# Optimization experiments

Measured on AMD Instinct MI355X. Metric: run time of the kernel, lower is better.

## Reference

```python
import jax, jax.numpy as jnp
import numpy as np

L_LAYERS = 4
N_HEAD = 16
D_MODEL = 1024
D_K = 64
D_V = 64
D_HID = 4096
D_OUT = 10000
SEQ = 512
BATCH = 16
MASK_RATE = 0.15
LN_EPS = 1e-5


def sinusoid_table(n_position, model_size):
    pos = np.arange(n_position)[:, None]
    hid = np.arange(model_size)[None, :]
    angle = pos / np.power(10000, 2 * (hid // 2) / model_size)
    tab = np.array(angle)
    tab[:, 0::2] = np.sin(tab[:, 0::2])
    tab[:, 1::2] = np.cos(tab[:, 1::2])
    return jnp.asarray(tab, dtype=jnp.float32)


def layer_norm(x, w, b):
    mu = jnp.mean(x, axis=-1, keepdims=True)
    var = jnp.mean(jnp.square(x - mu), axis=-1, keepdims=True)
    return (x - mu) * jax.lax.rsqrt(var + LN_EPS) * w + b


def setup_inputs() -> dict:
    key = jax.random.key(0)
    ks = jax.random.split(key, 32)
    s = 0.02
    inp = {
        "x": jax.random.normal(ks[0], (SEQ, BATCH, D_MODEL), dtype=jnp.float32),
        "rnd": jax.random.uniform(ks[1], (BATCH, SEQ), dtype=jnp.float32),
        "posi": sinusoid_table(SEQ, D_MODEL),
        "ln0_w": jnp.ones((D_MODEL,), jnp.float32),
        "ln0_b": jnp.zeros((D_MODEL,), jnp.float32),
        # stacked per-layer params [L, ...]
        "Wq": jax.random.normal(ks[2], (L_LAYERS, N_HEAD * D_K, D_MODEL), jnp.float32) * np.sqrt(2.0 / (D_MODEL + D_K)),
        "bq": jnp.zeros((L_LAYERS, N_HEAD * D_K), jnp.float32),
        "Wk": jax.random.normal(ks[3], (L_LAYERS, N_HEAD * D_K, D_MODEL), jnp.float32) * np.sqrt(2.0 / (D_MODEL + D_K)),
        "bk": jnp.zeros((L_LAYERS, N_HEAD * D_K), jnp.float32),
        "Wv": jax.random.normal(ks[4], (L_LAYERS, N_HEAD * D_V, D_MODEL), jnp.float32) * np.sqrt(2.0 / (D_MODEL + D_V)),
        "bv": jnp.zeros((L_LAYERS, N_HEAD * D_V), jnp.float32),
        "Wfc": jax.random.normal(ks[5], (L_LAYERS, D_MODEL, N_HEAD * D_V), jnp.float32) * s,
        "bfc": jnp.zeros((L_LAYERS, D_MODEL), jnp.float32),
        "ln1_w": jnp.ones((L_LAYERS, D_MODEL), jnp.float32),
        "ln1_b": jnp.zeros((L_LAYERS, D_MODEL), jnp.float32),
        "W1": jax.random.normal(ks[6], (L_LAYERS, D_HID, D_MODEL), jnp.float32) * s,
        "b1": jnp.zeros((L_LAYERS, D_HID), jnp.float32),
        "W2": jax.random.normal(ks[7], (L_LAYERS, D_MODEL, D_HID), jnp.float32) * s,
        "b2": jnp.zeros((L_LAYERS, D_MODEL), jnp.float32),
        "ln2_w": jnp.ones((L_LAYERS, D_MODEL), jnp.float32),
        "ln2_b": jnp.zeros((L_LAYERS, D_MODEL), jnp.float32),
        "Wo": jax.random.normal(ks[8], (D_OUT, D_MODEL), jnp.float32) * s,
        "bo": jnp.zeros((D_OUT,), jnp.float32),
    }
    return inp


def reference(x, rnd, posi, ln0_w, ln0_b, Wq, bq, Wk, bk, Wv, bv, Wfc, bfc,
              ln1_w, ln1_b, W1, b1, W2, b2, ln2_w, ln2_b, Wo, bo):
    scale = 1.0 / np.sqrt(D_K)
    # [length, batch, d] -> [batch, length, d]
    h = jnp.transpose(x, (1, 0, 2))
    # random input masking: keep where rnd > mask_rate
    keep = (rnd > MASK_RATE).astype(h.dtype)  # [B, S]
    h = h * keep[:, :, None]
    enc = layer_norm(h, ln0_w, ln0_b) + posi[None, :, :]

    for l in range(L_LAYERS):
        residual = enc
        q = (enc @ Wq[l].T + bq[l]).reshape(BATCH, SEQ, N_HEAD, D_K)
        k = (enc @ Wk[l].T + bk[l]).reshape(BATCH, SEQ, N_HEAD, D_K)
        v = (enc @ Wv[l].T + bv[l]).reshape(BATCH, SEQ, N_HEAD, D_V)
        attn = jnp.einsum('bqhd,bkhd->bhqk', q, k) * scale
        attn = jax.nn.softmax(attn, axis=-1)
        out = jnp.einsum('bhqk,bkhd->bqhd', attn, v).reshape(BATCH, SEQ, N_HEAD * D_V)
        out = out @ Wfc[l].T + bfc[l]
        enc = layer_norm(out + residual, ln1_w[l], ln1_b[l])
        # position-wise FFN (conv1d kernel=1 == per-token linear)
        ff = jax.nn.relu(enc @ W1[l].T + b1[l]) @ W2[l].T + b2[l]
        enc = layer_norm(ff + enc, ln2_w[l], ln2_b[l])

    logits = enc @ Wo.T + bo  # [B, S, D_OUT]
    out = jax.nn.log_softmax(logits, axis=-1)
    return jnp.transpose(out, (1, 0, 2))  # [S, B, D_OUT]
```

## Files before the change

### kernel.cpp

```cpp
#include <hip/hip_runtime.h>
#include <cstdint>

typedef unsigned short u16;
typedef unsigned int u32;
typedef __attribute__((ext_vector_type(8))) short vs8;
typedef __attribute__((ext_vector_type(4))) short vs4;
typedef __attribute__((ext_vector_type(4))) float vf4;
typedef __attribute__((ext_vector_type(4))) float f32x4;

#define NLAYER 4
#define SEQ 512
#define BATCH 16
#define DM 1024
#define NTOK 8192
#define DOUT 10000
#define DOUTP 10240

static __device__ __forceinline__ u16 f2bf(float f) {
    u32 u = __float_as_uint(f);
    return (u16)((u + 0x7FFFu + ((u >> 16) & 1u)) >> 16);
}
static __device__ __forceinline__ float bf2f(u16 h) { return __uint_as_float((u32)h << 16); }

static __device__ __forceinline__ void gload16(const void* g, void* l) {
    __builtin_amdgcn_global_load_lds(
        (const __attribute__((address_space(1))) u32*)(uintptr_t)g,
        (__attribute__((address_space(3))) u32*)(u32)(uintptr_t)l, 16, 0, 0);
}

template <int BM, bool RELU, bool OUTBF, bool TRV = false>
__global__ __launch_bounds__(512, 1) void gemm2p(const u16* __restrict__ A, const u16* __restrict__ Bw,
                                                 const float* __restrict__ bias, void* __restrict__ Cv,
                                                 int N, int K, int nMt, int nNt)
{
    constexpr int LA = BM / 128;
    constexpr int LB = 2;
    constexpr int WCNT = 2 * (LA + LB);
    constexpr int MR = BM / 32;

    __shared__ __align__(16) u16 lds[2 * 2 * BM * 32 + 2 * 2 * 256 * 32];
    u16* As = lds;
    u16* Bs = lds + 2 * 2 * BM * 32;

    const int t = threadIdx.x;
    const int wid = t >> 6, lane = t & 63;
    const int lr = lane & 15, lg = lane >> 4;
    const int wr = wid >> 2, wc = wid & 3;
    const int wrb = wr * (BM / 2), wcb = wc * 64;
    const int slot8 = (lg ^ ((lr >> 1) & 3)) * 8;

    const int nwg = nMt * nNt;
    const int orig = blockIdx.x;
    const int q8 = nwg >> 3, r8 = nwg & 7;
    const int xcd = orig & 7, idx = orig >> 3;
    const int wg = ((xcd < r8) ? xcd * (q8 + 1) : r8 * (q8 + 1) + (xcd - r8) * q8) + idx;
    const int GN = 8;
    const int gsz = GN * nMt;
    const int grp = wg / gsz;
    const int rem = wg - grp * gsz;
    const int gw = min(GN, nNt - grp * GN);
    const int mt = rem / gw;
    const int nt = grp * GN + (rem - mt * gw);
    const size_t m0 = (size_t)mt * BM;
    const size_t n0 = (size_t)nt * 256;

    const int srow = wid * 16 + (lane >> 2);
    const int scg = (lane & 3) ^ ((lane >> 3) & 3);
    const u16* gA = A + (m0 + srow) * (size_t)K + scg * 8;
    const u16* gB = Bw + (n0 + srow) * (size_t)K + scg * 8;

    auto stageA = [&](int b, int kh, int kt) {
#pragma unroll
        for (int i = 0; i < LA; ++i)
            gload16(gA + (size_t)i * 128 * K + kt + kh * 32,
                    &As[(((b << 1) + kh) * BM + (i * 8 + wid) * 16) * 32]);
    };
    auto stageB = [&](int b, int kh, int kt) {
#pragma unroll
        for (int i = 0; i < LB; ++i)
            gload16(gB + (size_t)i * 128 * K + kt + kh * 32,
                    &Bs[(((b << 1) + kh) * 256 + (i * 8 + wid) * 16) * 32]);
    };
    auto ldA = [&](int i, int kk, int b) -> vs8 {
        return *(const vs8*)&As[(((b << 1) + kk) * BM + wrb + i * 16 + lr) * 32 + slot8];
    };
    auto ldB = [&](int j, int kk, int b) -> vs8 {
        return *(const vs8*)&Bs[(((b << 1) + kk) * 256 + wcb + j * 16 + lr) * 32 + slot8];
    };

    f32x4 acc[MR][4];
#pragma unroll
    for (int i = 0; i < MR; ++i)
#pragma unroll
        for (int j = 0; j < 4; ++j) acc[i][j] = (f32x4){0.f, 0.f, 0.f, 0.f};

    const int NT = K >> 6;

    stageA(0, 0, 0); stageB(0, 0, 0);
    stageA(0, 1, 0); stageB(0, 1, 0);
    stageA(1, 0, 64); stageB(1, 0, 64);
    if constexpr (WCNT == 8) asm volatile("s_waitcnt vmcnt(8)" ::: "memory");
    else                     asm volatile("s_waitcnt vmcnt(6)" ::: "memory");
    __builtin_amdgcn_s_barrier();

    for (int tt = 0; tt < NT; ++tt) {
        const int buf = tt & 1;
        const int ktn = min(tt + 1, NT - 1) << 6;
        const int ktn2 = min(tt + 2, NT - 1) << 6;
        vs8 af[MR], bf[4];

#pragma unroll
        for (int j = 0; j < 4; ++j) bf[j] = ldB(j, 0, buf);
#pragma unroll
        for (int i = 0; i < MR; ++i) af[i] = ldA(i, 0, buf);
        stageA(buf ^ 1, 1, ktn);
        stageB(buf ^ 1, 1, ktn);
        __builtin_amdgcn_s_barrier();
        asm volatile("s_waitcnt lgkmcnt(0)" ::: "memory");
        __builtin_amdgcn_sched_barrier(0);
        __builtin_amdgcn_s_setprio(1);
#pragma unroll
        for (int i = 0; i < MR; ++i)
#pragma unroll
            for (int j = 0; j < 4; ++j) {
                if constexpr (TRV)
                    acc[i][j] = __builtin_amdgcn_mfma_f32_16x16x32_bf16(af[i], bf[j], acc[i][j], 0, 0, 0);
                else
                    acc[i][j] = __builtin_amdgcn_mfma_f32_16x16x32_bf16(bf[j], af[i], acc[i][j], 0, 0, 0);
            }
        __builtin_amdgcn_s_setprio(0);
        if constexpr (WCNT == 8) asm volatile("s_waitcnt vmcnt(8)" ::: "memory");
        else                     asm volatile("s_waitcnt vmcnt(6)" ::: "memory");
        __builtin_amdgcn_s_barrier();

#pragma unroll
        for (int j = 0; j < 4; ++j) bf[j] = ldB(j, 1, buf);
#pragma unroll
        for (int i = 0; i < MR; ++i) af[i] = ldA(i, 1, buf);
        stageA(buf, 0, ktn2);
        stageB(buf, 0, ktn2);
        __builtin_amdgcn_s_barrier();
        asm volatile("s_waitcnt lgkmcnt(0)" ::: "memory");
        __builtin_amdgcn_sched_barrier(0);
        __builtin_amdgcn_s_setprio(1);
#pragma unroll
        for (int i = 0; i < MR; ++i)
#pragma unroll
            for (int j = 0; j < 4; ++j) {
                if constexpr (TRV)
                    acc[i][j] = __builtin_amdgcn_mfma_f32_16x16x32_bf16(af[i], bf[j], acc[i][j], 0, 0, 0);
                else
                    acc[i][j] = __builtin_amdgcn_mfma_f32_16x16x32_bf16(bf[j], af[i], acc[i][j], 0, 0, 0);
            }
        __builtin_amdgcn_s_setprio(0);
        if constexpr (WCNT == 8) asm volatile("s_waitcnt vmcnt(8)" ::: "memory");
        else                     asm volatile("s_waitcnt vmcnt(6)" ::: "memory");
        __builtin_amdgcn_s_barrier();
    }

    asm volatile("s_waitcnt vmcnt(0)" ::: "memory");

    if constexpr (TRV) {
#pragma unroll
        for (int i = 0; i < MR; ++i) {
            const int cm0 = (int)m0 + wrb + 16 * i + lg * 4;
            const int b_ = cm0 >> 9, s_ = cm0 & 511;
#pragma unroll
            for (int j = 0; j < 4; ++j) {
                const int cn = (int)n0 + wcb + 16 * j + lr;
                const float bval = bias[cn];
                vs4 o;
#pragma unroll
                for (int r = 0; r < 4; ++r) o[r] = (short)f2bf(acc[i][j][r] + bval);
                u16* dst = (u16*)Cv + (((size_t)(b_ * 16 + (cn >> 6))) * 64 + (cn & 63)) * 512 + s_;
                *(vs4*)dst = o;
            }
        }
    } else {
#pragma unroll
        for (int i = 0; i < MR; ++i) {
            const size_t cm = m0 + wrb + 16 * i + lr;
#pragma unroll
            for (int j = 0; j < 4; ++j) {
                const size_t cn = n0 + wcb + 16 * j + lg * 4;
                const vf4 bv4 = *(const vf4*)&bias[cn];
                f32x4 v = acc[i][j];
#pragma unroll
                for (int r = 0; r < 4; ++r) {
                    v[r] += bv4[r];
                    if (RELU) v[r] = fmaxf(v[r], 0.f);
                }
                if (OUTBF) {
                    vs4 o;
#pragma unroll
                    for (int r = 0; r < 4; ++r) o[r] = (short)f2bf(v[r]);
                    *(vs4*)&((u16*)Cv)[cm * (size_t)N + cn] = o;
                } else {
                    *(vf4*)&((float*)Cv)[cm * (size_t)N + cn] = v;
                }
            }
        }
    }
}

__global__ __launch_bounds__(256) void attn_k(const u16* __restrict__ qb, const u16* __restrict__ kb,
                                              const u16* __restrict__ vtb, u16* __restrict__ ob, int ldq)
{
    __shared__ __align__(16) float SlF[32 * 520];
    const int t = threadIdx.x;
    const int wid = t >> 6, lane = t & 63;
    const int lr = lane & 15, lg = lane >> 4;
    const int bh = blockIdx.x >> 4, qt = blockIdx.x & 15;
    const int b = bh >> 4, h = bh & 15;
    const int q0 = qt * 32;

    vs8 aq[2][2];
#pragma unroll
    for (int i2 = 0; i2 < 2; ++i2)
#pragma unroll
        for (int kk = 0; kk < 2; ++kk)
            aq[i2][kk] = *(const vs8*)(qb + ((size_t)(b * 512 + q0 + 16 * i2 + lr)) * ldq + h * 64 + kk * 32 + lg * 8);

    f32x4 sa[2][8];
#pragma unroll
    for (int i2 = 0; i2 < 2; ++i2)
#pragma unroll
        for (int j = 0; j < 8; ++j) sa[i2][j] = (f32x4){0.f, 0.f, 0.f, 0.f};

#pragma unroll
    for (int j = 0; j < 8; ++j) {
        const int col = 128 * wid + 16 * j + lr;
#pragma unroll
        for (int kk = 0; kk < 2; ++kk) {
            vs8 bk = *(const vs8*)(kb + ((size_t)(b * 512 + col)) * ldq + h * 64 + kk * 32 + lg * 8);
#pragma unroll
            for (int i2 = 0; i2 < 2; ++i2)
                sa[i2][j] = __builtin_amdgcn_mfma_f32_16x16x32_bf16(bk, aq[i2][kk], sa[i2][j], 0, 0, 0);
        }
    }
#pragma unroll
    for (int i2 = 0; i2 < 2; ++i2)
#pragma unroll
        for (int j = 0; j < 8; ++j) {
            vf4 w;
#pragma unroll
            for (int r = 0; r < 4; ++r) w[r] = sa[i2][j][r] * 0.125f;
            *(vf4*)&SlF[(16 * i2 + lr) * 520 + 128 * wid + 16 * j + 4 * lg] = w;
        }
    __syncthreads();

    {
        const int row = t >> 3, seg = t & 7;
        const float* Sr = &SlF[row * 520 + seg * 64];
        float v[64];
        float m = -3.0e38f;
#pragma unroll
        for (int c = 0; c < 16; ++c) {
            const int cc = (c + row + seg) & 15;
            const vf4 w = *(const vf4*)&Sr[cc * 4];
#pragma unroll
            for (int e = 0; e < 4; ++e) { v[c * 4 + e] = w[e]; m = fmaxf(m, w[e]); }
        }
        m = fmaxf(m, __shfl_xor(m, 1));
        m = fmaxf(m, __shfl_xor(m, 2));
        m = fmaxf(m, __shfl_xor(m, 4));
        float s = 0.f;
#pragma unroll
        for (int i = 0; i < 64; ++i) { v[i] = __expf(v[i] - m); s += v[i]; }
        s += __shfl_xor(s, 1);
        s += __shfl_xor(s, 2);
        s += __shfl_xor(s, 4);
        const float inv = 1.f / s;
        u16* P16 = (u16*)SlF;
#pragma unroll
        for (int c = 0; c < 16; ++c) {
            const int cc = (c + row + seg) & 15;
            vs4 o;
#pragma unroll
            for (int e = 0; e < 4; ++e) o[e] = (short)f2bf(v[c * 4 + e] * inv);
            *(vs4*)&P16[row * 1040 + seg * 64 + cc * 4] = o;
        }
    }
    __syncthreads();

    const int rt = wid >> 1, ct0 = (wid & 1) * 2;
    f32x4 oa[2];
    oa[0] = (f32x4){0.f, 0.f, 0.f, 0.f};
    oa[1] = (f32x4){0.f, 0.f, 0.f, 0.f};
    const u16* P16 = (const u16*)SlF;
#pragma unroll
    for (int kt = 0; kt < 16; ++kt) {
        vs8 pa = *(const vs8*)&P16[(16 * rt + lr) * 1040 + kt * 32 + lg * 8];
#pragma unroll
        for (int c = 0; c < 2; ++c) {
            const int col = (ct0 + c) * 16 + lr;
            vs8 bv = *(const vs8*)(vtb + ((size_t)bh * 64 + col) * 512 + kt * 32 + lg * 8);
            oa[c] = __builtin_amdgcn_mfma_f32_16x16x32_bf16(bv, pa, oa[c], 0, 0, 0);
        }
    }
#pragma unroll
    for (int c = 0; c < 2; ++c) {
        const int qq = q0 + 16 * rt + lr;
        const int d0c = h * 64 + (ct0 + c) * 16 + lg * 4;
        vs4 o;
#pragma unroll
        for (int r = 0; r < 4; ++r) o[r] = (short)f2bf(oa[c][r]);
        *(vs4*)&ob[((size_t)b * 512 + qq) * 1024 + d0c] = o;
    }
}

__global__ __launch_bounds__(256) void embed_k(const float* __restrict__ x, const float* __restrict__ rnd,
                                               const float* __restrict__ posi, const float* __restrict__ w,
                                               const float* __restrict__ bb, u16* __restrict__ outb)
{
    const int tok = blockIdx.x;
    const int b = tok >> 9, s = tok & 511;
    const int t = threadIdx.x;
    const float keep = rnd[tok] > 0.15f ? 1.f : 0.f;
    vf4 xv = ((const vf4*)(x + ((size_t)s * 16 + b) * 1024))[t];
    xv *= keep;
    float s1 = xv[0] + xv[1] + xv[2] + xv[3];
    float s2 = xv[0] * xv[0] + xv[1] * xv[1] + xv[2] * xv[2] + xv[3] * xv[3];
#pragma unroll
    for (int mk = 1; mk < 64; mk <<= 1) { s1 += __shfl_xor(s1, mk); s2 += __shfl_xor(s2, mk); }
    __shared__ float red[8];
    if ((t & 63) == 0) { red[t >> 6] = s1; red[4 + (t >> 6)] = s2; }
    __syncthreads();
    s1 = red[0] + red[1] + red[2] + red[3];
    s2 = red[4] + red[5] + red[6] + red[7];
    const float mu = s1 * (1.f / 1024.f);
    const float var = s2 * (1.f / 1024.f) - mu * mu;
    const float rs = rsqrtf(var + 1e-5f);
    vf4 wv = ((const vf4*)w)[t];
    vf4 bv = ((const vf4*)bb)[t];
    vf4 pv = ((const vf4*)(posi + (size_t)s * 1024))[t];
    vs4 yb;
#pragma unroll
    for (int c = 0; c < 4; ++c)
        yb[c] = (short)f2bf((xv[c] - mu) * rs * wv[c] + bv[c] + pv[c]);
    *(vs4*)(outb + (size_t)tok * 1024 + t * 4) = yb;
}

__global__ __launch_bounds__(256) void add_ln_k(const u16* x, const u16* resid,
                                                const float* __restrict__ w, const float* __restrict__ bb,
                                                u16* out)
{
    const size_t row = blockIdx.x;
    const int t = threadIdx.x;
    const vs4 xv4 = *(const vs4*)(x + row * 1024 + t * 4);
    const vs4 rv4 = *(const vs4*)(resid + row * 1024 + t * 4);
    float xv[4];
#pragma unroll
    for (int c = 0; c < 4; ++c) xv[c] = bf2f((u16)xv4[c]) + bf2f((u16)rv4[c]);
    float s1 = xv[0] + xv[1] + xv[2] + xv[3];
    float s2 = xv[0] * xv[0] + xv[1] * xv[1] + xv[2] * xv[2] + xv[3] * xv[3];
#pragma unroll
    for (int mk = 1; mk < 64; mk <<= 1) { s1 += __shfl_xor(s1, mk); s2 += __shfl_xor(s2, mk); }
    __shared__ float red[8];
    if ((t & 63) == 0) { red[t >> 6] = s1; red[4 + (t >> 6)] = s2; }
    __syncthreads();
    s1 = red[0] + red[1] + red[2] + red[3];
    s2 = red[4] + red[5] + red[6] + red[7];
    const float mu = s1 * (1.f / 1024.f);
    const float var = s2 * (1.f / 1024.f) - mu * mu;
    const float rs = rsqrtf(var + 1e-5f);
    const vf4 wv = ((const vf4*)w)[t];
    const vf4 bv = ((const vf4*)bb)[t];
    vs4 yb;
#pragma unroll
    for (int c = 0; c < 4; ++c)
        yb[c] = (short)f2bf((xv[c] - mu) * rs * wv[c] + bv[c]);
    *(vs4*)(out + row * 1024 + t * 4) = yb;
}

__global__ __launch_bounds__(256) void logsm_k(const u16* __restrict__ lgts, float* __restrict__ out)
{
    const int tok = blockIdx.x;
    const int b = tok >> 9, s = tok & 511;
    const int t = threadIdx.x;
    const vs4* row4 = (const vs4*)(lgts + (size_t)tok * DOUTP);
    float v[40];
    float m = -3.0e38f;
#pragma unroll
    for (int i = 0; i < 10; ++i) {
        const int g = t + 256 * i;
        const vs4 x4 = __builtin_nontemporal_load(row4 + g);
#pragma unroll
        for (int e = 0; e < 4; ++e) {
            const float f = (g < 2500) ? bf2f((u16)x4[e]) : -3.0e38f;
            v[i * 4 + e] = f;
            m = fmaxf(m, f);
        }
    }
#pragma unroll
    for (int mk = 1; mk < 64; mk <<= 1) m = fmaxf(m, __shfl_xor(m, mk));
    __shared__ float red[8];
    if ((t & 63) == 0) red[t >> 6] = m;
    __syncthreads();
    m = fmaxf(fmaxf(red[0], red[1]), fmaxf(red[2], red[3]));
    float sum = 0.f;
#pragma unroll
    for (int i = 0; i < 40; ++i) { v[i] = __expf(v[i] - m); sum += v[i]; }
#pragma unroll
    for (int mk = 1; mk < 64; mk <<= 1) sum += __shfl_xor(sum, mk);
    if ((t & 63) == 0) red[4 + (t >> 6)] = sum;
    __syncthreads();
    sum = red[4] + red[5] + red[6] + red[7];
    const float ls = m + __logf(sum);
    vf4* orow = (vf4*)(out + ((size_t)s * 16 + b) * DOUT);
#pragma unroll
    for (int i = 0; i < 10; ++i) {
        const int g = t + 256 * i;
        if (g < 2500) {
            vf4 o;
#pragma unroll
            for (int e = 0; e < 4; ++e) o[e] = __logf(v[i * 4 + e]);
            const float adj = m - ls;
#pragma unroll
            for (int e = 0; e < 4; ++e) o[e] = o[e] + adj;
            __builtin_nontemporal_store(o, orow + g);
        }
    }
}

__global__ void prep_k(const float* __restrict__ Wq, const float* __restrict__ Wk,
                       const float* __restrict__ Wv, const float* __restrict__ Wfc,
                       const float* __restrict__ W1, const float* __restrict__ W2,
                       const float* __restrict__ Wo, const float* __restrict__ bq,
                       const float* __restrict__ bk, const float* __restrict__ bo,
                       u16* __restrict__ Wqk_b, u16* __restrict__ Wv_b, u16* __restrict__ Wfc_b,
                       u16* __restrict__ W1_b, u16* __restrict__ W2_b, u16* __restrict__ Wo_b,
                       float* __restrict__ bqk_p, float* __restrict__ bo_p)
{
    const int i = blockIdx.x * 256 + threadIdx.x;
    auto cvt = [](vf4 v) {
        vs4 o;
#pragma unroll
        for (int c = 0; c < 4; ++c) o[c] = (short)f2bf(v[c]);
        return o;
    };
    if (i < 1048576) {
        const int l = i >> 18, r = i & 262143;
        ((vs4*)Wqk_b)[(size_t)l * 524288 + r] = cvt(((const vf4*)Wq)[i]);
    } else if (i < 2097152) {
        const int ii = i - 1048576;
        const int l = ii >> 18, r = ii & 262143;
        ((vs4*)Wqk_b)[(size_t)l * 524288 + 262144 + r] = cvt(((const vf4*)Wk)[ii]);
    } else if (i < 3145728) {
        const int ii = i - 2097152;
        ((vs4*)Wv_b)[ii] = cvt(((const vf4*)Wv)[ii]);
    } else if (i < 4194304) {
        const int ii = i - 3145728;
        ((vs4*)Wfc_b)[ii] = cvt(((const vf4*)Wfc)[ii]);
    } else if (i < 8388608) {
        const int ii = i - 4194304;
        ((vs4*)W1_b)[ii] = cvt(((const vf4*)W1)[ii]);
    } else if (i < 12582912) {
        const int ii = i - 8388608;
        ((vs4*)W2_b)[ii] = cvt(((const vf4*)W2)[ii]);
    } else if (i < 15204352) {
        const int ii = i - 12582912;
        const size_t e = (size_t)ii * 4;
        const int r = (int)(e >> 10);
        vs4 o;
        if (r < DOUT) o = cvt(*(const vf4*)(Wo + (size_t)r * 1024 + (e & 1023)));
        else { o[0] = o[1] = o[2] = o[3] = 0; }
        *(vs4*)(Wo_b + e) = o;
    } else {
        const int ii = i - 15204352;
        if (ii < 2048) {
            const int f = ii * 4, l = f >> 11, c = f & 2047;
            vf4 v = (c < 1024) ? *(const vf4*)&bq[l * 1024 + c]
                               : *(const vf4*)&bk[l * 1024 + c - 1024];
            *(vf4*)&bqk_p[f] = v;
        } else {
            const int f = (ii - 2048) * 4;
            vf4 o;
#pragma unroll
            for (int e = 0; e < 4; ++e) o[e] = (f + e < DOUT) ? bo[f + e] : 0.f;
            *(vf4*)&bo_p[f] = o;
        }
    }
}

extern "C" void kernel_launch(void* const* d_in, const int* in_sizes, int n_in,
                              void* d_out, int out_size, void* d_ws, size_t ws_size,
                              hipStream_t stream)
{
    (void)in_sizes; (void)n_in; (void)out_size; (void)ws_size;
    const float* x     = (const float*)d_in[0];
    const float* rnd   = (const float*)d_in[1];
    const float* posi  = (const float*)d_in[2];
    const float* ln0_w = (const float*)d_in[3];
    const float* ln0_b = (const float*)d_in[4];
    const float* Wq    = (const float*)d_in[5];
    const float* bq    = (const float*)d_in[6];
    const float* Wk    = (const float*)d_in[7];
    const float* bk    = (const float*)d_in[8];
    const float* Wv    = (const float*)d_in[9];
    const float* bv    = (const float*)d_in[10];
    const float* Wfc   = (const float*)d_in[11];
    const float* bfc   = (const float*)d_in[12];
    const float* ln1_w = (const float*)d_in[13];
    const float* ln1_b = (const float*)d_in[14];
    const float* W1    = (const float*)d_in[15];
    const float* b1    = (const float*)d_in[16];
    const float* W2    = (const float*)d_in[17];
    const float* b2    = (const float*)d_in[18];
    const float* ln2_w = (const float*)d_in[19];
    const float* ln2_b = (const float*)d_in[20];
    const float* Wo    = (const float*)d_in[21];
    const float* bo    = (const float*)d_in[22];

    char* p = (char*)d_ws;
    size_t off = 0;
    auto take = [&](size_t bytes) {
        char* r = p + off;
        off += (bytes + 255) & ~(size_t)255;
        return r;
    };
    u16*   Wqk_b  = (u16*)take((size_t)NLAYER * 2048 * 1024 * 2);
    u16*   Wv_b   = (u16*)take((size_t)NLAYER * 1024 * 1024 * 2);
    u16*   Wfc_b  = (u16*)take((size_t)NLAYER * 1024 * 1024 * 2);
    u16*   W1_b   = (u16*)take((size_t)NLAYER * 4096 * 1024 * 2);
    u16*   W2_b   = (u16*)take((size_t)NLAYER * 4096 * 1024 * 2);
    u16*   Wo_b   = (u16*)take((size_t)DOUTP * DM * 2);
    float* bqk_p  = (float*)take(NLAYER * 2048 * 4);
    float* bo_p   = (float*)take(DOUTP * 4);
    u16*   enc_b  = (u16*)take((size_t)NTOK * DM * 2);
    char*  pool   = take((size_t)NTOK * DOUTP * 2);
    u16*   qkv_b  = (u16*)(pool);
    u16*   vt_b   = (u16*)(pool + 33554432);
    u16*   attn_b = (u16*)(pool + 50331648);
    u16*   fc_b   = (u16*)(pool);
    u16*   ff_b   = (u16*)(pool);
    u16*   ff2_b  = (u16*)(pool + 67108864);
    u16*   lgt_b  = (u16*)(pool);

    const dim3 blk(256);
    prep_k<<<59410, blk, 0, stream>>>(Wq, Wk, Wv, Wfc, W1, W2, Wo, bq, bk, bo,
                                      Wqk_b, Wv_b, Wfc_b, W1_b, W2_b, Wo_b, bqk_p, bo_p);

    embed_k<<<NTOK, blk, 0, stream>>>(x, rnd, posi, ln0_w, ln0_b, enc_b);

    const size_t l2e = 4096 * 1024;
    for (int l = 0; l < NLAYER; ++l) {
        gemm2p<256, false, true><<<256, 512, 0, stream>>>(enc_b, Wqk_b + (size_t)l * 2097152,
                                                          bqk_p + l * 2048, qkv_b, 2048, 1024, 32, 8);
        gemm2p<128, false, true, true><<<256, 512, 0, stream>>>(enc_b, Wv_b + (size_t)l * 1048576,
                                                                bv + l * 1024, vt_b, 1024, 1024, 64, 4);
        attn_k<<<4096, blk, 0, stream>>>(qkv_b, qkv_b + 1024, vt_b, attn_b, 2048);
        gemm2p<128, false, true><<<256, 512, 0, stream>>>(attn_b, Wfc_b + (size_t)l * 1048576,
                                                          bfc + l * 1024, fc_b, 1024, 1024, 64, 4);
        add_ln_k<<<NTOK, blk, 0, stream>>>(fc_b, enc_b, ln1_w + l * 1024, ln1_b + l * 1024, enc_b);
        gemm2p<256, true, true><<<512, 512, 0, stream>>>(enc_b, W1_b + l * l2e, b1 + l * 4096,
                                                         ff_b, 4096, 1024, 32, 16);
        gemm2p<128, false, true><<<256, 512, 0, stream>>>(ff_b, W2_b + l * l2e, b2 + l * 1024,
                                                          ff2_b, 1024, 4096, 64, 4);
        add_ln_k<<<NTOK, blk, 0, stream>>>(ff2_b, enc_b, ln2_w + l * 1024, ln2_b + l * 1024, enc_b);
    }

    gemm2p<256, false, true><<<1280, 512, 0, stream>>>(enc_b, Wo_b, bo_p, lgt_b, DOUTP, 1024, 32, 40);
    logsm_k<<<NTOK, blk, 0, stream>>>(lgt_b, (float*)d_out);
}
```

Baseline: 1.955 ms.

## Replace GEMM with 128x256 triple-buffered kernel, split-K for narrow GEMMs

The two-phase double-buffered GEMM with BM up to 256 becomes a single kernel with a fixed 128x256 tile, a 3-deep ring of K=32 slices, and launch bounds that allow up to 4 blocks per CU. The Wfc and W2 GEMMs (N=1024) now use split-K by 2, writing fp32 partials. A new add2_ln_k kernel sums the partials, bias and residual before layernorm. The aim is more blocks for occupancy and latency hiding on the small-N GEMMs. In exchange it adds extra fp32 partial traffic and smaller tiles with less reuse for the large GEMMs.

```diff
diff --git a/kernel.cpp b/kernel.cpp
--- a/kernel.cpp
+++ b/kernel.cpp
@@ -28,99 +28,85 @@
         (__attribute__((address_space(3))) u32*)(u32)(uintptr_t)l, 16, 0, 0);
 }
 
-template <int BM, bool RELU, bool OUTBF, bool TRV = false>
-__global__ __launch_bounds__(512, 1) void gemm2p(const u16* __restrict__ A, const u16* __restrict__ Bw,
+template <int NSP, bool RELU, bool OUTBF, bool TRV = false>
+__global__ __launch_bounds__(512, 4) void gemm1p(const u16* __restrict__ A, const u16* __restrict__ Bw,
                                                  const float* __restrict__ bias, void* __restrict__ Cv,
                                                  int N, int K, int nMt, int nNt)
 {
-    constexpr int LA = BM / 128;
-    constexpr int LB = 2;
-    constexpr int WCNT = 2 * (LA + LB);
-    constexpr int MR = BM / 32;
-
-    __shared__ __align__(16) u16 lds[2 * 2 * BM * 32 + 2 * 2 * 256 * 32];
+    __shared__ __align__(16) u16 lds[3 * 128 * 32 + 3 * 256 * 32];
     u16* As = lds;
-    u16* Bs = lds + 2 * 2 * BM * 32;
+    u16* Bs = lds + 3 * 128 * 32;
 
     const int t = threadIdx.x;
     const int wid = t >> 6, lane = t & 63;
     const int lr = lane & 15, lg = lane >> 4;
     const int wr = wid >> 2, wc = wid & 3;
-    const int wrb = wr * (BM / 2), wcb = wc * 64;
+    const int wrb = wr * 64, wcb = wc * 64;
     const int slot8 = (lg ^ ((lr >> 1) & 3)) * 8;
 
-    const int nwg = nMt * nNt;
+    const int nMtE = nMt * NSP;
+    const int nwg = nMtE * nNt;
     const int orig = blockIdx.x;
     const int q8 = nwg >> 3, r8 = nwg & 7;
     const int xcd = orig & 7, idx = orig >> 3;
     const int wg = ((xcd < r8) ? xcd * (q8 + 1) : r8 * (q8 + 1) + (xcd - r8) * q8) + idx;
     const int GN = 8;
-    const int gsz = GN * nMt;
+    const int gsz = GN * nMtE;
     const int grp = wg / gsz;
     const int rem = wg - grp * gsz;
     const int gw = min(GN, nNt - grp * GN);
-    const int mt = rem / gw;
-    const int nt = grp * GN + (rem - mt * gw);
-    const size_t m0 = (size_t)mt * BM;
+    const int mtE = rem / gw;
+    const int nt = grp * GN + (rem - mtE * gw);
+    const int spl = mtE / nMt;
+    const int mt = mtE - spl * nMt;
+    const size_t m0 = (size_t)mt * 128;
     const size_t n0 = (size_t)nt * 256;
+
+    const int KS = K / NSP;
+    const int NT = KS >> 5;
+    const int k0 = spl * KS;
 
     const int srow = wid * 16 + (lane >> 2);
     const int scg = (lane & 3) ^ ((lane >> 3) & 3);
-    const u16* gA = A + (m0 + srow) * (size_t)K + scg * 8;
-    const u16* gB = Bw + (n0 + srow) * (size_t)K + scg * 8;
-
-    auto stageA = [&](int b, int kh, int kt) {
-#pragma unroll
-        for (int i = 0; i < LA; ++i)
-            gload16(gA + (size_t)i * 128 * K + kt + kh * 32,
-                    &As[(((b << 1) + kh) * BM + (i * 8 + wid) * 16) * 32]);
+    const u16* gA = A + (m0 + srow) * (size_t)K + k0 + scg * 8;
+    const u16* gB = Bw + (n0 + srow) * (size_t)K + k0 + scg * 8;
+    u16* dA = &As[(wid * 16) * 32];
+    u16* dB = &Bs[(wid * 16) * 32];
+    const u16* rdA = &As[(wrb + lr) * 32 + slot8];
+    const u16* rdB = &Bs[(wcb + lr) * 32 + slot8];
+
+    auto stage = [&](int ring, int kt) {
+        gload16(gA + kt, dA + ring * 4096);
+        gload16(gB + kt, dB + ring * 8192);
+        gload16(gB + (size_t)128 * K + kt, dB + ring * 8192 + 4096);
     };
-    auto stageB = [&](int b, int kh, int kt) {
-#pragma unroll
-        for (int i = 0; i < LB; ++i)
-            gload16(gB + (size_t)i * 128 * K + kt + kh * 32,
-                    &Bs[(((b << 1) + kh) * 256 + (i * 8 + wid) * 16) * 32]);
-    };
-    auto ldA = [&](int i, int kk, int b) -> vs8 {
-        return *(const vs8*)&As[(((b << 1) + kk) * BM + wrb + i * 16 + lr) * 32 + slot8];
-    };
-    auto ldB = [&](int j, int kk, int b) -> vs8 {
-        return *(const vs8*)&Bs[(((b << 1) + kk) * 256 + wcb + j * 16 + lr) * 32 + slot8];
-    };
-
-    f32x4 acc[MR][4];
-#pragma unroll
-    for (int i = 0; i < MR; ++i)
+
+    f32x4 acc[4][4];
+#pragma unroll
+    for (int i = 0; i < 4; ++i)
 #pragma unroll
         for (int j = 0; j < 4; ++j) acc[i][j] = (f32x4){0.f, 0.f, 0.f, 0.f};
 
-    const int NT = K >> 6;
-
-    stageA(0, 0, 0); stageB(0, 0, 0);
-    stageA(0, 1, 0); stageB(0, 1, 0);
-    stageA(1, 0, 64); stageB(1, 0, 64);
-    if constexpr (WCNT == 8) asm volatile("s_waitcnt vmcnt(8)" ::: "memory");
-    else                     asm volatile("s_waitcnt vmcnt(6)" ::: "memory");
+    stage(0, 0);
+    stage(1, (NT > 1 ? 32 : 0));
+    asm volatile("s_waitcnt vmcnt(3)" ::: "memory");
     __builtin_amdgcn_s_barrier();
 
+    int ring = 0;
     for (int tt = 0; tt < NT; ++tt) {
-        const int buf = tt & 1;
-        const int ktn = min(tt + 1, NT - 1) << 6;
-        const int ktn2 = min(tt + 2, NT - 1) << 6;
-        vs8 af[MR], bf[4];
-
-#pragma unroll
-        for (int j = 0; j < 4; ++j) bf[j] = ldB(j, 0, buf);
-#pragma unroll
-        for (int i = 0; i < MR; ++i) af[i] = ldA(i, 0, buf);
-        stageA(buf ^ 1, 1, ktn);
-        stageB(buf ^ 1, 1, ktn);
-        __builtin_amdgcn_s_barrier();
+        int ring2 = ring + 2; if (ring2 >= 3) ring2 -= 3;
+        vs8 af[4], bf[4];
+#pragma unroll
+        for (int j = 0; j < 4; ++j) bf[j] = *(const vs8*)(rdB + ring * 8192 + j * 512);
+#pragma unroll
+        for (int i = 0; i < 4; ++i) af[i] = *(const vs8*)(rdA + ring * 4096 + i * 512);
+        const int ktn2 = min(tt + 2, NT - 1) << 5;
+        stage(ring2, ktn2);
         asm volatile("s_waitcnt lgkmcnt(0)" ::: "memory");
         __builtin_amdgcn_sched_barrier(0);
         __builtin_amdgcn_s_setprio(1);
 #pragma unroll
-        for (int i = 0; i < MR; ++i)
+        for (int i = 0; i < 4; ++i)
 #pragma unroll
             for (int j = 0; j < 4; ++j) {
                 if constexpr (TRV)
@@ -129,40 +115,16 @@
                     acc[i][j] = __builtin_amdgcn_mfma_f32_16x16x32_bf16(bf[j], af[i], acc[i][j], 0, 0, 0);
             }
         __builtin_amdgcn_s_setprio(0);
-        if constexpr (WCNT == 8) asm volatile("s_waitcnt vmcnt(8)" ::: "memory");
-        else                     asm volatile("s_waitcnt vmcnt(6)" ::: "memory");
+        asm volatile("s_waitcnt vmcnt(3)" ::: "memory");
         __builtin_amdgcn_s_barrier();
-
-#pragma unroll
-        for (int j = 0; j < 4; ++j) bf[j] = ldB(j, 1, buf);
-#pragma unroll
-        for (int i = 0; i < MR; ++i) af[i] = ldA(i, 1, buf);
-        stageA(buf, 0, ktn2);
-        stageB(buf, 0, ktn2);
-        __builtin_amdgcn_s_barrier();
-        asm volatile("s_waitcnt lgkmcnt(0)" ::: "memory");
-        __builtin_amdgcn_sched_barrier(0);
-        __builtin_amdgcn_s_setprio(1);
-#pragma unroll
-        for (int i = 0; i < MR; ++i)
-#pragma unroll
-            for (int j = 0; j < 4; ++j) {
-                if constexpr (TRV)
-                    acc[i][j] = __builtin_amdgcn_mfma_f32_16x16x32_bf16(af[i], bf[j], acc[i][j], 0, 0, 0);
-                else
-                    acc[i][j] = __builtin_amdgcn_mfma_f32_16x16x32_bf16(bf[j], af[i], acc[i][j], 0, 0, 0);
-            }
-        __builtin_amdgcn_s_setprio(0);
-        if constexpr (WCNT == 8) asm volatile("s_waitcnt vmcnt(8)" ::: "memory");
-        else                     asm volatile("s_waitcnt vmcnt(6)" ::: "memory");
-        __builtin_amdgcn_s_barrier();
+        ++ring; if (ring == 3) ring = 0;
     }
 
     asm volatile("s_waitcnt vmcnt(0)" ::: "memory");
 
     if constexpr (TRV) {
 #pragma unroll
-        for (int i = 0; i < MR; ++i) {
+        for (int i = 0; i < 4; ++i) {
             const int cm0 = (int)m0 + wrb + 16 * i + lg * 4;
             const int b_ = cm0 >> 9, s_ = cm0 & 511;
 #pragma unroll
@@ -176,28 +138,34 @@
                 *(vs4*)dst = o;
             }
         }
-    } else {
-#pragma unroll
-        for (int i = 0; i < MR; ++i) {
+    } else if constexpr (OUTBF) {
+#pragma unroll
+        for (int i = 0; i < 4; ++i) {
             const size_t cm = m0 + wrb + 16 * i + lr;
 #pragma unroll
             for (int j = 0; j < 4; ++j) {
                 const size_t cn = n0 + wcb + 16 * j + lg * 4;
                 const vf4 bv4 = *(const vf4*)&bias[cn];
                 f32x4 v = acc[i][j];
+                vs4 o;
 #pragma unroll
                 for (int r = 0; r < 4; ++r) {
-                    v[r] += bv4[r];
-                    if (RELU) v[r] = fmaxf(v[r], 0.f);
+                    float x = v[r] + bv4[r];
+                    if (RELU) x = fmaxf(x, 0.f);
+                    o[r] = (short)f2bf(x);
                 }
-                if (OUTBF) {
-                    vs4 o;
-#pragma unroll
-                    for (int r = 0; r < 4; ++r) o[r] = (short)f2bf(v[r]);
-                    *(vs4*)&((u16*)Cv)[cm * (size_t)N + cn] = o;
-                } else {
-                    *(vf4*)&((float*)Cv)[cm * (size_t)N + cn] = v;
-                }
+                *(vs4*)&((u16*)Cv)[cm * (size_t)N + cn] = o;
+            }
+        }
+    } else {
+        const size_t partOff = (size_t)spl * ((size_t)nMt * 128) * (size_t)N;
+#pragma unroll
+        for (int i = 0; i < 4; ++i) {
+            const size_t cm = m0 + wrb + 16 * i + lr;
+#pragma unroll
+            for (int j = 0; j < 4; ++j) {
+                const size_t cn = n0 + wcb + 16 * j + lg * 4;
+                *(vf4*)&((float*)Cv)[partOff + cm * (size_t)N + cn] = acc[i][j];
             }
         }
     }
@@ -373,6 +341,41 @@
     *(vs4*)(out + row * 1024 + t * 4) = yb;
 }
 
+__global__ __launch_bounds__(256) void add2_ln_k(const float* __restrict__ p0, const float* __restrict__ p1,
+                                                 const float* __restrict__ gb, const u16* resid,
+                                                 const float* __restrict__ w, const float* __restrict__ bb,
+                                                 u16* out)
+{
+    const size_t row = blockIdx.x;
+    const int t = threadIdx.x;
+    const vf4 a0 = ((const vf4*)(p0 + row * 1024))[t];
+    const vf4 a1 = ((const vf4*)(p1 + row * 1024))[t];
+    const vf4 g = ((const vf4*)gb)[t];
+    const vs4 rv4 = *(const vs4*)(resid + row * 1024 + t * 4);
+    float xv[4];
+#pragma unroll
+    for (int c = 0; c < 4; ++c) xv[c] = a0[c] + a1[c] + g[c] + bf2f((u16)rv4[c]);
+    float s1 = xv[0] + xv[1] + xv[2] + xv[3];
+    float s2 = xv[0] * xv[0] + xv[1] * xv[1] + xv[2] * xv[2] + xv[3] * xv[3];
+#pragma unroll
+    for (int mk = 1; mk < 64; mk <<= 1) { s1 += __shfl_xor(s1, mk); s2 += __shfl_xor(s2, mk); }
+    __shared__ float red[8];
+    if ((t & 63) == 0) { red[t >> 6] = s1; red[4 + (t >> 6)] = s2; }
+    __syncthreads();
+    s1 = red[0] + red[1] + red[2] + red[3];
+    s2 = red[4] + red[5] + red[6] + red[7];
+    const float mu = s1 * (1.f / 1024.f);
+    const float var = s2 * (1.f / 1024.f) - mu * mu;
+    const float rs = rsqrtf(var + 1e-5f);
+    const vf4 wv = ((const vf4*)w)[t];
+    const vf4 bv = ((const vf4*)bb)[t];
+    vs4 yb;
+#pragma unroll
+    for (int c = 0; c < 4; ++c)
+        yb[c] = (short)f2bf((xv[c] - mu) * rs * wv[c] + bv[c]);
+    *(vs4*)(out + row * 1024 + t * 4) = yb;
+}
+
 __global__ __launch_bounds__(256) void logsm_k(const u16* __restrict__ lgts, float* __restrict__ out)
 {
     const int tok = blockIdx.x;
@@ -407,6 +410,7 @@
     __syncthreads();
     sum = red[4] + red[5] + red[6] + red[7];
     const float ls = m + __logf(sum);
+    const float adj = m - ls;
     vf4* orow = (vf4*)(out + ((size_t)s * 16 + b) * DOUT);
 #pragma unroll
     for (int i = 0; i < 10; ++i) {
@@ -414,10 +418,7 @@
         if (g < 2500) {
             vf4 o;
 #pragma unroll
-            for (int e = 0; e < 4; ++e) o[e] = __logf(v[i * 4 + e]);
-            const float adj = m - ls;
-#pragma unroll
-            for (int e = 0; e < 4; ++e) o[e] = o[e] + adj;
+            for (int e = 0; e < 4; ++e) o[e] = __logf(v[i * 4 + e]) + adj;
             __builtin_nontemporal_store(o, orow + g);
         }
     }
@@ -529,12 +530,14 @@
     float* bo_p   = (float*)take(DOUTP * 4);
     u16*   enc_b  = (u16*)take((size_t)NTOK * DM * 2);
     char*  pool   = take((size_t)NTOK * DOUTP * 2);
-    u16*   qkv_b  = (u16*)(pool);
-    u16*   vt_b   = (u16*)(pool + 33554432);
-    u16*   attn_b = (u16*)(pool + 50331648);
-    u16*   fc_b   = (u16*)(pool);
+    u16*   attn_b = (u16*)(pool);
+    u16*   qkv_b  = (u16*)(pool + 16777216);
+    u16*   vt_b   = (u16*)(pool + 50331648);
+    float* fcp0   = (float*)(pool + 16777216);
+    float* fcp1   = (float*)(pool + 50331648);
     u16*   ff_b   = (u16*)(pool);
-    u16*   ff2_b  = (u16*)(pool + 67108864);
+    float* w2p0   = (float*)(pool + 67108864);
+    float* w2p1   = (float*)(pool + 100663296);
     u16*   lgt_b  = (u16*)(pool);
 
     const dim3 blk(256);
@@ -543,23 +546,24 @@
 
     embed_k<<<NTOK, blk, 0, stream>>>(x, rnd, posi, ln0_w, ln0_b, enc_b);
 
-    const size_t l2e = 4096 * 1024;
     for (int l = 0; l < NLAYER; ++l) {
-        gemm2p<256, false, true><<<256, 512, 0, stream>>>(enc_b, Wqk_b + (size_t)l * 2097152,
-                                                          bqk_p + l * 2048, qkv_b, 2048, 1024, 32, 8);
-        gemm2p<128, false, true, true><<<256, 512, 0, stream>>>(enc_b, Wv_b + (size_t)l * 1048576,
-                                                                bv + l * 1024, vt_b, 1024, 1024, 64, 4);
+        gemm1p<1, false, true><<<512, 512, 0, stream>>>(enc_b, Wqk_b + (size_t)l * 2097152,
+                                                        bqk_p + l * 2048, qkv_b, 2048, 1024, 64, 8);
+        gemm1p<1, false, true, true><<<256, 512, 0, stream>>>(enc_b, Wv_b + (size_t)l * 1048576,
+                                                              bv + l * 1024, vt_b, 1024, 1024, 64, 4);
         attn_k<<<4096, blk, 0, stream>>>(qkv_b, qkv_b + 1024, vt_b, attn_b, 2048);
-        gemm2p<128, false, true><<<256, 512, 0, stream>>>(attn_b, Wfc_b + (size_t)l * 1048576,
-                                                          bfc + l * 1024, fc_b, 1024, 1024, 64, 4);
-        add_ln_k<<<NTOK, blk, 0, stream>>>(fc_b, enc_b, ln1_w + l * 1024, ln1_b + l * 1024, enc_b);
-        gemm2p<256, true, true><<<512, 512, 0, stream>>>(enc_b, W1_b + l * l2e, b1 + l * 4096,
-                                                         ff_b, 4096, 1024, 32, 16);
-        gemm2p<128, false, true><<<256, 512, 0, stream>>>(ff_b, W2_b + l * l2e, b2 + l * 1024,
-                                                          ff2_b, 1024, 4096, 64, 4);
-        add_ln_k<<<NTOK, blk, 0, stream>>>(ff2_b, enc_b, ln2_w + l * 1024, ln2_b + l * 1024, enc_b);
-    }
-
-    gemm2p<256, false, true><<<1280, 512, 0, stream>>>(enc_b, Wo_b, bo_p, lgt_b, DOUTP, 1024, 32, 40);
+        gemm1p<2, false, false><<<512, 512, 0, stream>>>(attn_b, Wfc_b + (size_t)l * 1048576,
+                                                         nullptr, fcp0, 1024, 1024, 64, 4);
+        add2_ln_k<<<NTOK, blk, 0, stream>>>(fcp0, fcp1, bfc + l * 1024, enc_b,
+                                            ln1_w + l * 1024, ln1_b + l * 1024, enc_b);
+        gemm1p<1, true, true><<<1024, 512, 0, stream>>>(enc_b, W1_b + (size_t)l * 4194304,
+                                                        b1 + l * 4096, ff_b, 4096, 1024, 64, 16);
+        gemm1p<2, false, false><<<512, 512, 0, stream>>>(ff_b, W2_b + (size_t)l * 4194304,
+                                                         nullptr, w2p0, 1024, 4096, 64, 4);
+        add2_ln_k<<<NTOK, blk, 0, stream>>>(w2p0, w2p1, b2 + l * 1024, enc_b,
+                                            ln2_w + l * 1024, ln2_b + l * 1024, enc_b);
+    }
+
+    gemm1p<1, false, true><<<2560, 512, 0, stream>>>(enc_b, Wo_b, bo_p, lgt_b, DOUTP, 1024, 64, 40);
     logsm_k<<<NTOK, blk, 0, stream>>>(lgt_b, (float*)d_out);
 }
```

After: 2.082 ms. 1.07x slower.
